# Optimization experiments

Measured on AMD Instinct MI355X. Metric: run time of the kernel, lower is better.

The kernel has to match this reference:

```python
import jax, jax.numpy as jnp
import numpy as np

NUMBASIS = 10
OFFSET = jnp.linspace(-3.0, 3.0, NUMBASIS)
COEFF = -0.5 / (OFFSET[1] - OFFSET[0]) ** 2
CR_CR_MEAN, CR_CR_STD = 4.0, 0.16
CR_I_MEAN, CR_I_STD = 2.8, 0.035
ANGLE_MEAN, ANGLE_STD = -0.025, 0.06

E, N, G = 1_000_000, 250_000, 512

def _rbf(x):
    # x: [E, 1] -> [E, NUMBASIS]; PyG GaussianSmearing
    d = x - OFFSET
    return jnp.exp(COEFF * d * d)

def _layernorm(x, g, b, eps=1e-5):
    mu = jnp.mean(x, axis=-1, keepdims=True)
    xc = x - mu
    var = jnp.mean(xc * xc, axis=-1, keepdims=True)
    return xc * jax.lax.rsqrt(var + eps) * g + b

def setup_inputs() -> dict:
    key = jax.random.key(0)
    ks = jax.random.split(key, 16)
    def w(k, shape):
        return jax.random.normal(k, shape, jnp.float32) / np.sqrt(shape[0])
    return {
        "edge_src": jax.random.randint(ks[0], (E,), 0, N),
        "edge_dst": jax.random.randint(ks[1], (E,), 0, N),
        "batch_idx": jnp.sort(jax.random.randint(ks[2], (N,), 0, G)),
        "cell": jax.random.normal(ks[3], (G, 3, 3), jnp.float32),
        "edge_shift": jax.random.normal(ks[4], (E, 3), jnp.float32),
        "pos": jax.random.normal(ks[5], (N, 3), jnp.float32),
        "angles": jax.random.normal(ks[6], (E,), jnp.float32),
        "cr_i_bonds": jax.random.normal(ks[7], (E, 4), jnp.float32),
        "ln_g": jnp.ones((60,), jnp.float32),
        "ln_b": jnp.zeros((60,), jnp.float32),
        "wn1": w(ks[8], (60, 32)), "bn1": jnp.zeros((32,), jnp.float32),
        "wn2": w(ks[9], (32, 1)), "bn2": jnp.zeros((1,), jnp.float32),
        "we1": w(ks[10], (60, 64)), "be1": jnp.zeros((64,), jnp.float32),
        "we2": w(ks[11], (64, 1)), "be2": jnp.zeros((1,), jnp.float32),
        "wr1": w(ks[12], (60, 32)), "br1": jnp.zeros((32,), jnp.float32),
        "wr2": w(ks[13], (32, 2)), "br2": jnp.zeros((2,), jnp.float32),
    }

def reference(edge_src, edge_dst, batch_idx, cell, edge_shift, pos, angles,
              cr_i_bonds, ln_g, ln_b, wn1, bn1, wn2, bn2, we1, be1, we2, be2,
              wr1, br1, wr2, br2):
    gidx = batch_idx[edge_src]                      # [E]
    bcell = cell[gidx]                              # [E,3,3]
    tvec = jnp.einsum('ei,eij->ej', edge_shift, bcell)
    radvec = pos[edge_dst] - pos[edge_src] + tvec   # [E,3]
    dist = jnp.linalg.norm(radvec, axis=1, keepdims=True)  # [E,1]
    ang = angles.reshape(-1, 1)
    dist_z = (dist - CR_CR_MEAN) / CR_CR_STD
    ang_z = (ang - ANGLE_MEAN) / ANGLE_STD
    legs_z = (cr_i_bonds - CR_I_MEAN) / CR_I_STD    # [E,4]
    emb = jnp.concatenate([
        _rbf(dist_z), _rbf(ang_z),
        _rbf(legs_z[:, 0:1]), _rbf(legs_z[:, 1:2]),
        _rbf(legs_z[:, 2:3]), _rbf(legs_z[:, 3:4]),
    ], axis=-1)                                     # [E,60]
    h = _layernorm(emb, ln_g, ln_b)
    # dropout layers are identity in eval mode
    routing = jax.nn.softmax(jax.nn.silu(h @ wr1 + br1) @ wr2 + br2, axis=-1)
    pred_normal = jax.nn.silu(h @ wn1 + bn1) @ wn2 + bn2   # [E,1]
    pred_extreme = jax.nn.silu(h @ we1 + be1) @ we2 + be2  # [E,1]
    out = routing[:, 0:1] * pred_normal + routing[:, 1:2] * pred_extreme
    return out.reshape(-1)
```

## Files before the change

### kernel.cpp

```cpp
#include <hip/hip_runtime.h>
#include <math.h>

#define E_THREADS 128
#define EPB 128

typedef __attribute__((ext_vector_type(8))) short short8;
typedef __attribute__((ext_vector_type(4))) float floatx4;


#define A_L2E 1.6230319f

__device__ inline unsigned short f2bf(float f) {
    union { float f; unsigned u; } v; v.f = f;
    unsigned r = v.u + 0x7FFFu + ((v.u >> 16) & 1u);
    return (unsigned short)(r >> 16);
}

__device__ inline unsigned cvt_pk_bf16(float lo, float hi) {
    unsigned r;
    asm("v_cvt_pk_bf16_f32 %0, %1, %2" : "=v"(r) : "v"(lo), "v"(hi));
    return r;
}

__device__ inline float fexp2(float x) { return __builtin_amdgcn_exp2f(x); }
__device__ inline float frcp(float x)  { return __builtin_amdgcn_rcpf(x); }
#define LOG2E 1.44269504f

__global__ __launch_bounds__(256)
void prep_weights(
    const float* __restrict__ ln_g, const float* __restrict__ ln_b,
    const float* __restrict__ wn1, const float* __restrict__ bn1,
    const float* __restrict__ wn2, const float* __restrict__ bn2,
    const float* __restrict__ we1, const float* __restrict__ be1,
    const float* __restrict__ we2, const float* __restrict__ be2,
    const float* __restrict__ wr1, const float* __restrict__ br1,
    const float* __restrict__ wr2, const float* __restrict__ br2,
    char* __restrict__ ws)
{
    uint4* WF  = (uint4*)ws;
    float* W2A = (float*)(ws + 16384);
    float* W2B = (float*)(ws + 16896);
    float* SC  = (float*)(ws + 17024);
    const int tid = threadIdx.x;

    for (int idx = tid; idx < 1024; idx += 256) {
        int u = idx >> 7, s = (idx >> 6) & 1, lane = idx & 63;
        int lcol = lane & 15, khi = lane >> 4;
        int n = 16 * u + lcol;
        int kbase = s * 32 + khi * 8;
        float w8[8];
        for (int j = 0; j < 8; ++j) {
            int k = kbase + j;
            float w = 0.0f;
            if (k < 60) {
                float wv = (n < 32) ? wn1[k * 32 + n]
                         : (n < 96) ? we1[k * 64 + (n - 32)]
                                    : wr1[k * 32 + (n - 96)];
                w = ln_g[k] * wv;
            } else if (k == 60) {
                float b = (n < 32) ? bn1[n] : (n < 96) ? be1[n - 32] : br1[n - 96];
                for (int kk = 0; kk < 60; ++kk) {
                    float wv = (n < 32) ? wn1[kk * 32 + n]
                             : (n < 96) ? we1[kk * 64 + (n - 32)]
                                        : wr1[kk * 32 + (n - 96)];
                    b += ln_b[kk] * wv;
                }
                w = b;
            }
            w8[j] = w;
        }
        unsigned q0 = (unsigned)f2bf(w8[0]) | ((unsigned)f2bf(w8[1]) << 16);
        unsigned q1 = (unsigned)f2bf(w8[2]) | ((unsigned)f2bf(w8[3]) << 16);
        unsigned q2 = (unsigned)f2bf(w8[4]) | ((unsigned)f2bf(w8[5]) << 16);
        unsigned q3 = (unsigned)f2bf(w8[6]) | ((unsigned)f2bf(w8[7]) << 16);
        WF[idx] = make_uint4(q0, q1, q2, q3);
    }
    if (tid < 128) {
        int n = tid;
        W2A[n] = (n < 32) ? wn2[n] : (n < 96) ? we2[n - 32] : wr2[(n - 96) * 2];
    }
    if (tid >= 128 && tid < 160) W2B[tid - 128] = wr2[(tid - 128) * 2 + 1];
    if (tid == 0) { SC[0] = bn2[0]; SC[1] = be2[0]; SC[2] = br2[0]; SC[3] = br2[1]; }
}

__global__ __launch_bounds__(E_THREADS)
void exchange_block_kernel(
    const int*   __restrict__ edge_src,
    const int*   __restrict__ edge_dst,
    const int*   __restrict__ batch_idx,
    const float* __restrict__ cell,
    const float* __restrict__ edge_shift,
    const float* __restrict__ pos,
    const float* __restrict__ angles,
    const float* __restrict__ cr_bonds,
    const char*  __restrict__ ws,
    float* __restrict__ out, int E)
{
    __shared__ __align__(16) unsigned short HLDS[EPB * 64];
    __shared__ __align__(16) float LW2A[128];
    __shared__ __align__(16) float LW2B[32];

    const int tid  = threadIdx.x;
    const int lane = tid & 63;
    const int wv   = tid >> 6;
    const int e = blockIdx.x * EPB + tid;

    LW2A[tid] = ((const float*)(ws + 16384))[tid];
    if (tid < 32) LW2B[tid] = ((const float*)(ws + 16896))[tid];

    float h[64];
    if (e < E) {
        int s = edge_src[e];
        int d = edge_dst[e];
        int g = batch_idx[s];
        float sh0 = edge_shift[e * 3 + 0];
        float sh1 = edge_shift[e * 3 + 1];
        float sh2 = edge_shift[e * 3 + 2];
        const float* c = cell + g * 9;
        float t0 = sh0 * c[0] + sh1 * c[3] + sh2 * c[6];
        float t1 = sh0 * c[1] + sh1 * c[4] + sh2 * c[7];
        float t2 = sh0 * c[2] + sh1 * c[5] + sh2 * c[8];
        float r0 = pos[d * 3 + 0] - pos[s * 3 + 0] + t0;
        float r1 = pos[d * 3 + 1] - pos[s * 3 + 1] + t1;
        float r2 = pos[d * 3 + 2] - pos[s * 3 + 2] + t2;
        float dist = sqrtf(r0 * r0 + r1 * r1 + r2 * r2);

        float z[6];
        z[0] = (dist - 4.0f) * (1.0f / 0.16f);
        z[1] = (angles[e] + 0.025f) * (1.0f / 0.06f);
        z[2] = (cr_bonds[e * 4 + 0] - 2.8f) * (1.0f / 0.035f);
        z[3] = (cr_bonds[e * 4 + 1] - 2.8f) * (1.0f / 0.035f);
        z[4] = (cr_bonds[e * 4 + 2] - 2.8f) * (1.0f / 0.035f);
        z[5] = (cr_bonds[e * 4 + 3] - 2.8f) * (1.0f / 0.035f);

        #pragma unroll
        for (int gi = 0; gi < 6; ++gi) {
            float zv = fminf(13.0f, fmaxf(-13.0f, z[gi]));
            float tt = zv + 3.0f;
            float hv = fexp2(-A_L2E * tt * tt);
            float rv = fexp2(fmaf(zv, 2.1640426f, 5.7707802f));
            h[gi * 10] = hv;
            #pragma unroll
            for (int k = 1; k < 10; ++k) {
                hv *= rv;
                rv *= 0.36787944f;
                h[gi * 10 + k] = hv;
            }
        }
        float mu = 0.0f;
        #pragma unroll
        for (int k = 0; k < 60; ++k) mu += h[k];
        mu *= (1.0f / 60.0f);
        float var = 0.0f;
        #pragma unroll
        for (int k = 0; k < 60; ++k) { float xc = h[k] - mu; var += xc * xc; }
        var *= (1.0f / 60.0f);
        float rs = rsqrtf(var + 1e-5f);
        float nmurs = -mu * rs;
        #pragma unroll
        for (int k = 0; k < 60; ++k) h[k] = fmaf(h[k], rs, nmurs);
    } else {
        #pragma unroll
        for (int k = 0; k < 60; ++k) h[k] = 0.0f;
    }
    h[60] = 1.0f;
    h[61] = 0.0f; h[62] = 0.0f; h[63] = 0.0f;

    {
        const int swz = (tid & 7) << 4;
        #pragma unroll
        for (int c = 0; c < 8; ++c) {
            unsigned q0 = cvt_pk_bf16(h[8 * c + 0], h[8 * c + 1]);
            unsigned q1 = cvt_pk_bf16(h[8 * c + 2], h[8 * c + 3]);
            unsigned q2 = cvt_pk_bf16(h[8 * c + 4], h[8 * c + 5]);
            unsigned q3 = cvt_pk_bf16(h[8 * c + 6], h[8 * c + 7]);
            *(uint4*)((char*)HLDS + tid * 128 + ((c * 16) ^ swz)) = make_uint4(q0, q1, q2, q3);
        }
    }
    __syncthreads();

    const short8* WF = (const short8*)ws;
    const float*  SC = (const float*)(ws + 17024);

    const int lcol = lane & 15;
    const int khi  = lane >> 4;
    const int kof  = khi * 16;

    short8 wf[16];
    #pragma unroll
    for (int i = 0; i < 16; ++i) wf[i] = WF[i * 64 + lane];

    const float bn2v = SC[0], be2v = SC[1], br2v0 = SC[2], br2v1 = SC[3];

    float val[4];
    #pragma unroll
    for (int t = 0; t < 4; ++t) {
        const int hrow = wv * 64 + t * 16 + lcol;
        const char* hbase = (const char*)HLDS + hrow * 128;
        const int hswz = (hrow & 7) << 4;
        short8 b0 = *(const short8*)(hbase + ((0  + kof) ^ hswz));
        short8 b1 = *(const short8*)(hbase + ((64 + kof) ^ hswz));

        float sN = 0.0f, sE = 0.0f, sR0 = 0.0f, sR1 = 0.0f;
        #pragma unroll
        for (int u = 0; u < 8; ++u) {
            short8 a0 = wf[u * 2 + 0];
            short8 a1 = wf[u * 2 + 1];
            floatx4 acc = (floatx4){0.f, 0.f, 0.f, 0.f};
            acc = __builtin_amdgcn_mfma_f32_16x16x32_bf16(a0, b0, acc, 0, 0, 0);
            acc = __builtin_amdgcn_mfma_f32_16x16x32_bf16(a1, b1, acc, 0, 0, 0);

            float4 w2 = *(const float4*)&LW2A[16 * u + khi * 4];
            const float* w2p = (const float*)&w2;
            float4 wb4;
            const float* wbp = (const float*)&wb4;
            if (u >= 6) wb4 = *(const float4*)&LW2B[(u - 6) * 16 + khi * 4];
            #pragma unroll
            for (int j = 0; j < 4; ++j) {
                float a  = acc[j];
                float sl = a * frcp(1.0f + fexp2(a * -LOG2E));
                float w  = w2p[j];
                if (u < 2)      sN += sl * w;
                else if (u < 6) sE += sl * w;
                else {
                    sR0 += sl * w;
                    sR1 += sl * wbp[j];
                }
            }
        }
        sN  += __shfl_xor(sN,  16); sN  += __shfl_xor(sN,  32);
        sE  += __shfl_xor(sE,  16); sE  += __shfl_xor(sE,  32);
        sR0 += __shfl_xor(sR0, 16); sR0 += __shfl_xor(sR0, 32);
        sR1 += __shfl_xor(sR1, 16); sR1 += __shfl_xor(sR1, 32);

        sN += bn2v; sE += be2v; sR0 += br2v0; sR1 += br2v1;
        float rt = frcp(1.0f + fexp2((sR1 - sR0) * LOG2E));
        val[t] = sE + rt * (sN - sE);
    }

    {
        float v = (khi == 0) ? val[0] : (khi == 1) ? val[1]
                : (khi == 2) ? val[2] : val[3];
        int eb = blockIdx.x * EPB + wv * 64 + khi * 16 + lcol;
        if (eb < E) out[eb] = v;
    }
}

extern "C" void kernel_launch(void* const* d_in, const int* in_sizes, int n_in,
                              void* d_out, int out_size, void* d_ws, size_t ws_size,
                              hipStream_t stream)
{
    const int*   edge_src  = (const int*)  d_in[0];
    const int*   edge_dst  = (const int*)  d_in[1];
    const int*   batch_idx = (const int*)  d_in[2];
    const float* cell      = (const float*)d_in[3];
    const float* edge_shift= (const float*)d_in[4];
    const float* pos       = (const float*)d_in[5];
    const float* angles    = (const float*)d_in[6];
    const float* cr_bonds  = (const float*)d_in[7];
    const float* ln_g      = (const float*)d_in[8];
    const float* ln_b      = (const float*)d_in[9];
    const float* wn1 = (const float*)d_in[10]; const float* bn1 = (const float*)d_in[11];
    const float* wn2 = (const float*)d_in[12]; const float* bn2 = (const float*)d_in[13];
    const float* we1 = (const float*)d_in[14]; const float* be1 = (const float*)d_in[15];
    const float* we2 = (const float*)d_in[16]; const float* be2 = (const float*)d_in[17];
    const float* wr1 = (const float*)d_in[18]; const float* br1 = (const float*)d_in[19];
    const float* wr2 = (const float*)d_in[20]; const float* br2 = (const float*)d_in[21];

    int E = in_sizes[0];
    float* out = (float*)d_out;

    hipLaunchKernelGGL(prep_weights, dim3(1), dim3(256), 0, stream,
                       ln_g, ln_b, wn1, bn1, wn2, bn2, we1, be1, we2, be2,
                       wr1, br1, wr2, br2, (char*)d_ws);

    int grid = (E + EPB - 1) / EPB;
    hipLaunchKernelGGL(exchange_block_kernel, dim3(grid), dim3(E_THREADS), 0, stream,
                       edge_src, edge_dst, batch_idx, cell, edge_shift, pos,
                       angles, cr_bonds, (const char*)d_ws, out, E);
}
```

Measured before the change: 94.01 us.

## Process multiple edge chunks per block with software-prefetched edge inputs

Each block now loops over four consecutive 128-edge chunks, prefetching the next chunk's edge indices, angles, bonds and shifts into registers while the current chunk runs through the MFMA MLP. Weight fragments are re-read from global/L1 inside the MFMA loop instead of being held in 16 registers, and occupancy hints (waves_per_eu, launch_bounds min blocks) are added to raise occupancy. The prep kernel uses 1024 threads with no loop. This amortizes block startup and LW2 staging and overlaps gather latency with compute, but it reduces grid parallelism by 4x and adds repeated weight loads and an extra barrier per chunk.

```diff
diff --git a/kernel.cpp b/kernel.cpp
--- a/kernel.cpp
+++ b/kernel.cpp
@@ -3,12 +3,14 @@
 
 #define E_THREADS 128
 #define EPB 128
+#define CPB 4
 
 typedef __attribute__((ext_vector_type(8))) short short8;
 typedef __attribute__((ext_vector_type(4))) float floatx4;
 
 
 #define A_L2E 1.6230319f
+#define LOG2E 1.44269504f
 
 __device__ inline unsigned short f2bf(float f) {
     union { float f; unsigned u; } v; v.f = f;
@@ -24,9 +26,8 @@
 
 __device__ inline float fexp2(float x) { return __builtin_amdgcn_exp2f(x); }
 __device__ inline float frcp(float x)  { return __builtin_amdgcn_rcpf(x); }
-#define LOG2E 1.44269504f
-
-__global__ __launch_bounds__(256)
+
+__global__ __launch_bounds__(1024)
 void prep_weights(
     const float* __restrict__ ln_g, const float* __restrict__ ln_b,
     const float* __restrict__ wn1, const float* __restrict__ bn1,
@@ -43,12 +44,14 @@
     float* SC  = (float*)(ws + 17024);
     const int tid = threadIdx.x;
 
-    for (int idx = tid; idx < 1024; idx += 256) {
+    {
+        int idx = tid;
         int u = idx >> 7, s = (idx >> 6) & 1, lane = idx & 63;
         int lcol = lane & 15, khi = lane >> 4;
         int n = 16 * u + lcol;
         int kbase = s * 32 + khi * 8;
         float w8[8];
+        #pragma unroll
         for (int j = 0; j < 8; ++j) {
             int k = kbase + j;
             float w = 0.0f;
@@ -59,6 +62,7 @@
                 w = ln_g[k] * wv;
             } else if (k == 60) {
                 float b = (n < 32) ? bn1[n] : (n < 96) ? be1[n - 32] : br1[n - 96];
+                #pragma unroll 4
                 for (int kk = 0; kk < 60; ++kk) {
                     float wv = (n < 32) ? wn1[kk * 32 + n]
                              : (n < 96) ? we1[kk * 64 + (n - 32)]
@@ -83,7 +87,8 @@
     if (tid == 0) { SC[0] = bn2[0]; SC[1] = be2[0]; SC[2] = br2[0]; SC[3] = br2[1]; }
 }
 
-__global__ __launch_bounds__(E_THREADS)
+__attribute__((amdgpu_waves_per_eu(4, 5)))
+__global__ __launch_bounds__(E_THREADS, 4)
 void exchange_block_kernel(
     const int*   __restrict__ edge_src,
     const int*   __restrict__ edge_dst,
@@ -103,146 +108,189 @@
     const int tid  = threadIdx.x;
     const int lane = tid & 63;
     const int wv   = tid >> 6;
-    const int e = blockIdx.x * EPB + tid;
-
-    LW2A[tid] = ((const float*)(ws + 16384))[tid];
-    if (tid < 32) LW2B[tid] = ((const float*)(ws + 16896))[tid];
-
-    float h[64];
-    if (e < E) {
-        int s = edge_src[e];
-        int d = edge_dst[e];
-        int g = batch_idx[s];
-        float sh0 = edge_shift[e * 3 + 0];
-        float sh1 = edge_shift[e * 3 + 1];
-        float sh2 = edge_shift[e * 3 + 2];
-        const float* c = cell + g * 9;
-        float t0 = sh0 * c[0] + sh1 * c[3] + sh2 * c[6];
-        float t1 = sh0 * c[1] + sh1 * c[4] + sh2 * c[7];
-        float t2 = sh0 * c[2] + sh1 * c[5] + sh2 * c[8];
-        float r0 = pos[d * 3 + 0] - pos[s * 3 + 0] + t0;
-        float r1 = pos[d * 3 + 1] - pos[s * 3 + 1] + t1;
-        float r2 = pos[d * 3 + 2] - pos[s * 3 + 2] + t2;
-        float dist = sqrtf(r0 * r0 + r1 * r1 + r2 * r2);
-
-        float z[6];
-        z[0] = (dist - 4.0f) * (1.0f / 0.16f);
-        z[1] = (angles[e] + 0.025f) * (1.0f / 0.06f);
-        z[2] = (cr_bonds[e * 4 + 0] - 2.8f) * (1.0f / 0.035f);
-        z[3] = (cr_bonds[e * 4 + 1] - 2.8f) * (1.0f / 0.035f);
-        z[4] = (cr_bonds[e * 4 + 2] - 2.8f) * (1.0f / 0.035f);
-        z[5] = (cr_bonds[e * 4 + 3] - 2.8f) * (1.0f / 0.035f);
-
-        #pragma unroll
-        for (int gi = 0; gi < 6; ++gi) {
-            float zv = fminf(13.0f, fmaxf(-13.0f, z[gi]));
-            float tt = zv + 3.0f;
-            float hv = fexp2(-A_L2E * tt * tt);
-            float rv = fexp2(fmaf(zv, 2.1640426f, 5.7707802f));
-            h[gi * 10] = hv;
-            #pragma unroll
-            for (int k = 1; k < 10; ++k) {
-                hv *= rv;
-                rv *= 0.36787944f;
-                h[gi * 10 + k] = hv;
-            }
-        }
-        float mu = 0.0f;
-        #pragma unroll
-        for (int k = 0; k < 60; ++k) mu += h[k];
-        mu *= (1.0f / 60.0f);
-        float var = 0.0f;
-        #pragma unroll
-        for (int k = 0; k < 60; ++k) { float xc = h[k] - mu; var += xc * xc; }
-        var *= (1.0f / 60.0f);
-        float rs = rsqrtf(var + 1e-5f);
-        float nmurs = -mu * rs;
-        #pragma unroll
-        for (int k = 0; k < 60; ++k) h[k] = fmaf(h[k], rs, nmurs);
-    } else {
-        #pragma unroll
-        for (int k = 0; k < 60; ++k) h[k] = 0.0f;
-    }
-    h[60] = 1.0f;
-    h[61] = 0.0f; h[62] = 0.0f; h[63] = 0.0f;
-
-    {
-        const int swz = (tid & 7) << 4;
-        #pragma unroll
-        for (int c = 0; c < 8; ++c) {
-            unsigned q0 = cvt_pk_bf16(h[8 * c + 0], h[8 * c + 1]);
-            unsigned q1 = cvt_pk_bf16(h[8 * c + 2], h[8 * c + 3]);
-            unsigned q2 = cvt_pk_bf16(h[8 * c + 4], h[8 * c + 5]);
-            unsigned q3 = cvt_pk_bf16(h[8 * c + 6], h[8 * c + 7]);
-            *(uint4*)((char*)HLDS + tid * 128 + ((c * 16) ^ swz)) = make_uint4(q0, q1, q2, q3);
-        }
-    }
-    __syncthreads();
-
-    const short8* WF = (const short8*)ws;
-    const float*  SC = (const float*)(ws + 17024);
-
     const int lcol = lane & 15;
     const int khi  = lane >> 4;
     const int kof  = khi * 16;
 
-    short8 wf[16];
-    #pragma unroll
-    for (int i = 0; i < 16; ++i) wf[i] = WF[i * 64 + lane];
-
+    LW2A[tid] = ((const float*)(ws + 16384))[tid];
+    if (tid < 32) LW2B[tid] = ((const float*)(ws + 16896))[tid];
+
+    const short8* WF = (const short8*)ws;
+    const float*  SC = (const float*)(ws + 17024);
     const float bn2v = SC[0], be2v = SC[1], br2v0 = SC[2], br2v1 = SC[3];
 
-    float val[4];
-    #pragma unroll
-    for (int t = 0; t < 4; ++t) {
-        const int hrow = wv * 64 + t * 16 + lcol;
-        const char* hbase = (const char*)HLDS + hrow * 128;
-        const int hswz = (hrow & 7) << 4;
-        short8 b0 = *(const short8*)(hbase + ((0  + kof) ^ hswz));
-        short8 b1 = *(const short8*)(hbase + ((64 + kof) ^ hswz));
-
-        float sN = 0.0f, sE = 0.0f, sR0 = 0.0f, sR1 = 0.0f;
+    const int nchunks = (E + EPB - 1) / EPB;
+    const int chunk0 = blockIdx.x * CPB;
+
+    int pe = chunk0 * EPB + tid;
+
+    int    pf_s = 0, pf_d = 0;
+    float  pf_ang = 0.0f, pf_sh0 = 0.0f, pf_sh1 = 0.0f, pf_sh2 = 0.0f;
+    float4 pf_bond = make_float4(0.f, 0.f, 0.f, 0.f);
+    if (pe < E) {
+        pf_s   = edge_src[pe];
+        pf_d   = edge_dst[pe];
+        pf_ang = angles[pe];
+        pf_bond = *(const float4*)(cr_bonds + pe * 4);
+        pf_sh0 = edge_shift[pe * 3 + 0];
+        pf_sh1 = edge_shift[pe * 3 + 1];
+        pf_sh2 = edge_shift[pe * 3 + 2];
+    }
+
+    for (int ci = 0; ci < CPB; ++ci) {
+        const int chunk = chunk0 + ci;
+        if (chunk >= nchunks) break;
+
+        float h[64];
+        if (pe < E) {
+            int s = pf_s, d = pf_d;
+            int g = batch_idx[s];
+            float pdx = pos[d * 3 + 0], pdy = pos[d * 3 + 1], pdz = pos[d * 3 + 2];
+            float psx = pos[s * 3 + 0], psy = pos[s * 3 + 1], psz = pos[s * 3 + 2];
+            const float* c = cell + g * 9;
+
+            float z1 = (pf_ang + 0.025f) * (1.0f / 0.06f);
+            float z2 = (pf_bond.x - 2.8f) * (1.0f / 0.035f);
+            float z3 = (pf_bond.y - 2.8f) * (1.0f / 0.035f);
+            float z4 = (pf_bond.z - 2.8f) * (1.0f / 0.035f);
+            float z5 = (pf_bond.w - 2.8f) * (1.0f / 0.035f);
+
+            float zarr[5] = {z1, z2, z3, z4, z5};
+            #pragma unroll
+            for (int gi = 1; gi < 6; ++gi) {
+                float zv = fminf(13.0f, fmaxf(-13.0f, zarr[gi - 1]));
+                float tt = zv + 3.0f;
+                float hv = fexp2(-A_L2E * tt * tt);
+                float rv = fexp2(fmaf(zv, 2.1640426f, 5.7707802f));
+                h[gi * 10] = hv;
+                #pragma unroll
+                for (int k = 1; k < 10; ++k) {
+                    hv *= rv;
+                    rv *= 0.36787944f;
+                    h[gi * 10 + k] = hv;
+                }
+            }
+
+            float t0 = pf_sh0 * c[0] + pf_sh1 * c[3] + pf_sh2 * c[6];
+            float t1 = pf_sh0 * c[1] + pf_sh1 * c[4] + pf_sh2 * c[7];
+            float t2 = pf_sh0 * c[2] + pf_sh1 * c[5] + pf_sh2 * c[8];
+            float r0 = pdx - psx + t0;
+            float r1 = pdy - psy + t1;
+            float r2 = pdz - psz + t2;
+            float dist = sqrtf(r0 * r0 + r1 * r1 + r2 * r2);
+            float z0 = (dist - 4.0f) * (1.0f / 0.16f);
+            {
+                float zv = fminf(13.0f, fmaxf(-13.0f, z0));
+                float tt = zv + 3.0f;
+                float hv = fexp2(-A_L2E * tt * tt);
+                float rv = fexp2(fmaf(zv, 2.1640426f, 5.7707802f));
+                h[0] = hv;
+                #pragma unroll
+                for (int k = 1; k < 10; ++k) {
+                    hv *= rv;
+                    rv *= 0.36787944f;
+                    h[k] = hv;
+                }
+            }
+
+            float mu = 0.0f;
+            #pragma unroll
+            for (int k = 0; k < 60; ++k) mu += h[k];
+            mu *= (1.0f / 60.0f);
+            float var = 0.0f;
+            #pragma unroll
+            for (int k = 0; k < 60; ++k) { float xc = h[k] - mu; var += xc * xc; }
+            var *= (1.0f / 60.0f);
+            float rs = rsqrtf(var + 1e-5f);
+            float nmurs = -mu * rs;
+            #pragma unroll
+            for (int k = 0; k < 60; ++k) h[k] = fmaf(h[k], rs, nmurs);
+        } else {
+            #pragma unroll
+            for (int k = 0; k < 60; ++k) h[k] = 0.0f;
+        }
+        h[60] = 1.0f;
+        h[61] = 0.0f; h[62] = 0.0f; h[63] = 0.0f;
+
+        __syncthreads();
+
+        {
+            const int swz = (tid & 7) << 4;
+            #pragma unroll
+            for (int cc = 0; cc < 8; ++cc) {
+                unsigned q0 = cvt_pk_bf16(h[8 * cc + 0], h[8 * cc + 1]);
+                unsigned q1 = cvt_pk_bf16(h[8 * cc + 2], h[8 * cc + 3]);
+                unsigned q2 = cvt_pk_bf16(h[8 * cc + 4], h[8 * cc + 5]);
+                unsigned q3 = cvt_pk_bf16(h[8 * cc + 6], h[8 * cc + 7]);
+                *(uint4*)((char*)HLDS + tid * 128 + ((cc * 16) ^ swz)) = make_uint4(q0, q1, q2, q3);
+            }
+        }
+        __syncthreads();
+
+        int pe2 = pe + EPB;
+        if (pe2 < E) {
+            pf_s   = edge_src[pe2];
+            pf_d   = edge_dst[pe2];
+            pf_ang = angles[pe2];
+            pf_bond = *(const float4*)(cr_bonds + pe2 * 4);
+            pf_sh0 = edge_shift[pe2 * 3 + 0];
+            pf_sh1 = edge_shift[pe2 * 3 + 1];
+            pf_sh2 = edge_shift[pe2 * 3 + 2];
+        }
+        pe = pe2;
+
+        float val[4];
         #pragma unroll
-        for (int u = 0; u < 8; ++u) {
-            short8 a0 = wf[u * 2 + 0];
-            short8 a1 = wf[u * 2 + 1];
-            floatx4 acc = (floatx4){0.f, 0.f, 0.f, 0.f};
-            acc = __builtin_amdgcn_mfma_f32_16x16x32_bf16(a0, b0, acc, 0, 0, 0);
-            acc = __builtin_amdgcn_mfma_f32_16x16x32_bf16(a1, b1, acc, 0, 0, 0);
-
-            float4 w2 = *(const float4*)&LW2A[16 * u + khi * 4];
-            const float* w2p = (const float*)&w2;
-            float4 wb4;
-            const float* wbp = (const float*)&wb4;
-            if (u >= 6) wb4 = *(const float4*)&LW2B[(u - 6) * 16 + khi * 4];
-            #pragma unroll
-            for (int j = 0; j < 4; ++j) {
-                float a  = acc[j];
-                float sl = a * frcp(1.0f + fexp2(a * -LOG2E));
-                float w  = w2p[j];
-                if (u < 2)      sN += sl * w;
-                else if (u < 6) sE += sl * w;
-                else {
-                    sR0 += sl * w;
-                    sR1 += sl * wbp[j];
+        for (int t = 0; t < 4; ++t) {
+            const int hrow = wv * 64 + t * 16 + lcol;
+            const char* hbase = (const char*)HLDS + hrow * 128;
+            const int hswz = (hrow & 7) << 4;
+            short8 b0 = *(const short8*)(hbase + ((0  + kof) ^ hswz));
+            short8 b1 = *(const short8*)(hbase + ((64 + kof) ^ hswz));
+
+            float sN = 0.0f, sE = 0.0f, sR0 = 0.0f, sR1 = 0.0f;
+            #pragma unroll
+            for (int u = 0; u < 8; ++u) {
+                short8 a0 = WF[(u * 2 + 0) * 64 + lane];
+                short8 a1 = WF[(u * 2 + 1) * 64 + lane];
+                floatx4 acc = (floatx4){0.f, 0.f, 0.f, 0.f};
+                acc = __builtin_amdgcn_mfma_f32_16x16x32_bf16(a0, b0, acc, 0, 0, 0);
+                acc = __builtin_amdgcn_mfma_f32_16x16x32_bf16(a1, b1, acc, 0, 0, 0);
+
+                float4 w2 = *(const float4*)&LW2A[16 * u + khi * 4];
+                const float* w2p = (const float*)&w2;
+                float4 wb4;
+                const float* wbp = (const float*)&wb4;
+                if (u >= 6) wb4 = *(const float4*)&LW2B[(u - 6) * 16 + khi * 4];
+                #pragma unroll
+                for (int j = 0; j < 4; ++j) {
+                    float a  = acc[j];
+                    float sl = a * frcp(1.0f + fexp2(a * -LOG2E));
+                    float w  = w2p[j];
+                    if (u < 2)      sN += sl * w;
+                    else if (u < 6) sE += sl * w;
+                    else {
+                        sR0 += sl * w;
+                        sR1 += sl * wbp[j];
+                    }
                 }
             }
-        }
-        sN  += __shfl_xor(sN,  16); sN  += __shfl_xor(sN,  32);
-        sE  += __shfl_xor(sE,  16); sE  += __shfl_xor(sE,  32);
-        sR0 += __shfl_xor(sR0, 16); sR0 += __shfl_xor(sR0, 32);
-        sR1 += __shfl_xor(sR1, 16); sR1 += __shfl_xor(sR1, 32);
-
-        sN += bn2v; sE += be2v; sR0 += br2v0; sR1 += br2v1;
-        float rt = frcp(1.0f + fexp2((sR1 - sR0) * LOG2E));
-        val[t] = sE + rt * (sN - sE);
-    }
-
-    {
-        float v = (khi == 0) ? val[0] : (khi == 1) ? val[1]
-                : (khi == 2) ? val[2] : val[3];
-        int eb = blockIdx.x * EPB + wv * 64 + khi * 16 + lcol;
-        if (eb < E) out[eb] = v;
+            sN  += __shfl_xor(sN,  16); sN  += __shfl_xor(sN,  32);
+            sE  += __shfl_xor(sE,  16); sE  += __shfl_xor(sE,  32);
+            sR0 += __shfl_xor(sR0, 16); sR0 += __shfl_xor(sR0, 32);
+            sR1 += __shfl_xor(sR1, 16); sR1 += __shfl_xor(sR1, 32);
+
+            sN += bn2v; sE += be2v; sR0 += br2v0; sR1 += br2v1;
+            float rt = frcp(1.0f + fexp2((sR1 - sR0) * LOG2E));
+            val[t] = sE + rt * (sN - sE);
+        }
+
+        {
+            float v = (khi == 0) ? val[0] : (khi == 1) ? val[1]
+                    : (khi == 2) ? val[2] : val[3];
+            int eb = chunk * EPB + wv * 64 + khi * 16 + lcol;
+            if (eb < E) out[eb] = v;
+        }
     }
 }
 
@@ -270,11 +318,12 @@
     int E = in_sizes[0];
     float* out = (float*)d_out;
 
-    hipLaunchKernelGGL(prep_weights, dim3(1), dim3(256), 0, stream,
+    hipLaunchKernelGGL(prep_weights, dim3(1), dim3(1024), 0, stream,
                        ln_g, ln_b, wn1, bn1, wn2, bn2, we1, be1, we2, be2,
                        wr1, br1, wr2, br2, (char*)d_ws);
 
-    int grid = (E + EPB - 1) / EPB;
+    int nchunks = (E + EPB - 1) / EPB;
+    int grid = (nchunks + CPB - 1) / CPB;
     hipLaunchKernelGGL(exchange_block_kernel, dim3(grid), dim3(E_THREADS), 0, stream,
                        edge_src, edge_dst, batch_idx, cell, edge_shift, pos,
                        angles, cr_bonds, (const char*)d_ws, out, E);
```

New measurement: 253.2 us. 169% more time.

## Fold layernorm normalization into GEMM via bias columns and post-scale

Applied to the files above, without the earlier changes.

Computes mean and variance in one pass while packing raw RBF values to bf16 directly, and drops the separate normalize pass. Normalization moves into the matmul: bias and sum(g*w) columns are added to the weights, the edge row carries sqrt(var) and -mu as extra inputs, and each accumulator is scaled by rsqrt(var) afterwards. This cuts register pressure, since the 64-float h array and the 16 preloaded weight fragments are gone and weights are now read inside the loop. The weight prep kernel uses 1024 threads with one element each. The one-pass variance and bf16 rounding of mu and sqrt(var) may reduce accuracy.

```diff
diff --git a/kernel.cpp b/kernel.cpp
--- a/kernel.cpp
+++ b/kernel.cpp
@@ -9,6 +9,7 @@
 
 
 #define A_L2E 1.6230319f
+#define LOG2E 1.44269504f
 
 __device__ inline unsigned short f2bf(float f) {
     union { float f; unsigned u; } v; v.f = f;
@@ -24,9 +25,8 @@
 
 __device__ inline float fexp2(float x) { return __builtin_amdgcn_exp2f(x); }
 __device__ inline float frcp(float x)  { return __builtin_amdgcn_rcpf(x); }
-#define LOG2E 1.44269504f
-
-__global__ __launch_bounds__(256)
+
+__global__ __launch_bounds__(1024)
 void prep_weights(
     const float* __restrict__ ln_g, const float* __restrict__ ln_b,
     const float* __restrict__ wn1, const float* __restrict__ bn1,
@@ -43,12 +43,14 @@
     float* SC  = (float*)(ws + 17024);
     const int tid = threadIdx.x;
 
-    for (int idx = tid; idx < 1024; idx += 256) {
+    {
+        int idx = tid;
         int u = idx >> 7, s = (idx >> 6) & 1, lane = idx & 63;
         int lcol = lane & 15, khi = lane >> 4;
         int n = 16 * u + lcol;
         int kbase = s * 32 + khi * 8;
         float w8[8];
+        #pragma unroll
         for (int j = 0; j < 8; ++j) {
             int k = kbase + j;
             float w = 0.0f;
@@ -66,6 +68,15 @@
                     b += ln_b[kk] * wv;
                 }
                 w = b;
+            } else if (k == 61) {
+                float sacc = 0.0f;
+                for (int kk = 0; kk < 60; ++kk) {
+                    float wv = (n < 32) ? wn1[kk * 32 + n]
+                             : (n < 96) ? we1[kk * 64 + (n - 32)]
+                                        : wr1[kk * 32 + (n - 96)];
+                    sacc += ln_g[kk] * wv;
+                }
+                w = sacc;
             }
             w8[j] = w;
         }
@@ -97,6 +108,7 @@
     float* __restrict__ out, int E)
 {
     __shared__ __align__(16) unsigned short HLDS[EPB * 64];
+    __shared__ __align__(16) float RSL[EPB];
     __shared__ __align__(16) float LW2A[128];
     __shared__ __align__(16) float LW2B[32];
 
@@ -108,7 +120,8 @@
     LW2A[tid] = ((const float*)(ws + 16384))[tid];
     if (tid < 32) LW2B[tid] = ((const float*)(ws + 16896))[tid];
 
-    float h[64];
+    unsigned p[32];
+    float rs = 0.0f;
     if (e < E) {
         int s = edge_src[e];
         int d = edge_dst[e];
@@ -133,48 +146,42 @@
         z[4] = (cr_bonds[e * 4 + 2] - 2.8f) * (1.0f / 0.035f);
         z[5] = (cr_bonds[e * 4 + 3] - 2.8f) * (1.0f / 0.035f);
 
+        float sum = 0.0f, sumsq = 0.0f;
         #pragma unroll
         for (int gi = 0; gi < 6; ++gi) {
             float zv = fminf(13.0f, fmaxf(-13.0f, z[gi]));
             float tt = zv + 3.0f;
             float hv = fexp2(-A_L2E * tt * tt);
             float rv = fexp2(fmaf(zv, 2.1640426f, 5.7707802f));
-            h[gi * 10] = hv;
+            float prev = hv;
+            sum += hv; sumsq = fmaf(hv, hv, sumsq);
             #pragma unroll
             for (int k = 1; k < 10; ++k) {
                 hv *= rv;
                 rv *= 0.36787944f;
-                h[gi * 10 + k] = hv;
+                sum += hv; sumsq = fmaf(hv, hv, sumsq);
+                if (k & 1) p[5 * gi + (k >> 1)] = cvt_pk_bf16(prev, hv);
+                else       prev = hv;
             }
         }
-        float mu = 0.0f;
-        #pragma unroll
-        for (int k = 0; k < 60; ++k) mu += h[k];
-        mu *= (1.0f / 60.0f);
-        float var = 0.0f;
-        #pragma unroll
-        for (int k = 0; k < 60; ++k) { float xc = h[k] - mu; var += xc * xc; }
-        var *= (1.0f / 60.0f);
-        float rs = rsqrtf(var + 1e-5f);
-        float nmurs = -mu * rs;
-        #pragma unroll
-        for (int k = 0; k < 60; ++k) h[k] = fmaf(h[k], rs, nmurs);
+        float mu  = sum * (1.0f / 60.0f);
+        float var = fmaxf(sumsq * (1.0f / 60.0f) - mu * mu, 0.0f) + 1e-5f;
+        rs = rsqrtf(var);
+        float inv = sqrtf(var);
+        p[30] = cvt_pk_bf16(inv, -mu);
+        p[31] = 0u;
     } else {
         #pragma unroll
-        for (int k = 0; k < 60; ++k) h[k] = 0.0f;
-    }
-    h[60] = 1.0f;
-    h[61] = 0.0f; h[62] = 0.0f; h[63] = 0.0f;
+        for (int k = 0; k < 32; ++k) p[k] = 0u;
+    }
+    RSL[tid] = rs;
 
     {
         const int swz = (tid & 7) << 4;
         #pragma unroll
-        for (int c = 0; c < 8; ++c) {
-            unsigned q0 = cvt_pk_bf16(h[8 * c + 0], h[8 * c + 1]);
-            unsigned q1 = cvt_pk_bf16(h[8 * c + 2], h[8 * c + 3]);
-            unsigned q2 = cvt_pk_bf16(h[8 * c + 4], h[8 * c + 5]);
-            unsigned q3 = cvt_pk_bf16(h[8 * c + 6], h[8 * c + 7]);
-            *(uint4*)((char*)HLDS + tid * 128 + ((c * 16) ^ swz)) = make_uint4(q0, q1, q2, q3);
+        for (int cc = 0; cc < 8; ++cc) {
+            *(uint4*)((char*)HLDS + tid * 128 + ((cc * 16) ^ swz)) =
+                make_uint4(p[4 * cc + 0], p[4 * cc + 1], p[4 * cc + 2], p[4 * cc + 3]);
         }
     }
     __syncthreads();
@@ -185,10 +192,6 @@
     const int lcol = lane & 15;
     const int khi  = lane >> 4;
     const int kof  = khi * 16;
-
-    short8 wf[16];
-    #pragma unroll
-    for (int i = 0; i < 16; ++i) wf[i] = WF[i * 64 + lane];
 
     const float bn2v = SC[0], be2v = SC[1], br2v0 = SC[2], br2v1 = SC[3];
 
@@ -200,12 +203,13 @@
         const int hswz = (hrow & 7) << 4;
         short8 b0 = *(const short8*)(hbase + ((0  + kof) ^ hswz));
         short8 b1 = *(const short8*)(hbase + ((64 + kof) ^ hswz));
+        const float rs_e = RSL[hrow];
 
         float sN = 0.0f, sE = 0.0f, sR0 = 0.0f, sR1 = 0.0f;
         #pragma unroll
         for (int u = 0; u < 8; ++u) {
-            short8 a0 = wf[u * 2 + 0];
-            short8 a1 = wf[u * 2 + 1];
+            short8 a0 = WF[(u * 2 + 0) * 64 + lane];
+            short8 a1 = WF[(u * 2 + 1) * 64 + lane];
             floatx4 acc = (floatx4){0.f, 0.f, 0.f, 0.f};
             acc = __builtin_amdgcn_mfma_f32_16x16x32_bf16(a0, b0, acc, 0, 0, 0);
             acc = __builtin_amdgcn_mfma_f32_16x16x32_bf16(a1, b1, acc, 0, 0, 0);
@@ -217,7 +221,7 @@
             if (u >= 6) wb4 = *(const float4*)&LW2B[(u - 6) * 16 + khi * 4];
             #pragma unroll
             for (int j = 0; j < 4; ++j) {
-                float a  = acc[j];
+                float a  = rs_e * acc[j];
                 float sl = a * frcp(1.0f + fexp2(a * -LOG2E));
                 float w  = w2p[j];
                 if (u < 2)      sN += sl * w;
@@ -270,7 +274,7 @@
     int E = in_sizes[0];
     float* out = (float*)d_out;
 
-    hipLaunchKernelGGL(prep_weights, dim3(1), dim3(256), 0, stream,
+    hipLaunchKernelGGL(prep_weights, dim3(1), dim3(1024), 0, stream,
                        ln_g, ln_b, wn1, bn1, wn2, bn2, we1, be1, we2, be2,
                        wr1, br1, wr2, br2, (char*)d_ws);
 
```

After: 89.54 us. -4.8%, faster.
